# Kernel tuning notes

Measured on AMD Instinct MI355X. Metric: run time of the kernel, lower is better.

Reference implementation:

```python
import jax, jax.numpy as jnp
import numpy as np

N = 50000      # nodes
E = 800000     # edges
F_IN = 128     # input features
H = 8          # heads
F = 16         # features per head
NEG_SLOPE = 0.2


def setup_inputs() -> dict:
    key = jax.random.key(0)
    k_x, k_ei, k_w, k_as, k_ad = jax.random.split(key, 5)
    x = jax.random.normal(k_x, (N, F_IN), dtype=jnp.float32)
    edge_index = jax.random.randint(k_ei, (2, E), 0, N, dtype=jnp.int64)
    # learned params (PyG GATConv: lin weight [H*F, F_in] no bias; att_src/att_dst [H, F]; out bias [H*F])
    glorot = lambda k, shp: jax.random.uniform(k, shp, jnp.float32, -1.0, 1.0) * np.sqrt(6.0 / (shp[-1] + shp[-2]))
    W = glorot(k_w, (H * F, F_IN))
    att_src = glorot(k_as, (H, F))
    att_dst = glorot(k_ad, (H, F))
    bias = jnp.zeros((H * F,), dtype=jnp.float32)  # bias_init = zeros_
    return {"x": x, "W": W, "att_src": att_src, "att_dst": att_dst, "bias": bias, "edge_index": edge_index}


def reference(x, W, att_src, att_dst, bias, edge_index):
    # linear projection, split heads: [N, H, F]
    h = (x @ W.T).reshape(N, H, F)
    # per-node attention logits: [N, H]
    a_src = jnp.einsum('nhf,hf->nh', h, att_src)
    a_dst = jnp.einsum('nhf,hf->nh', h, att_dst)
    src, dst = edge_index[0], edge_index[1]
    # edge scores + LeakyReLU: [E, H]
    e = a_src[src] + a_dst[dst]
    e = jnp.where(e >= 0, e, NEG_SLOPE * e)
    # segment softmax over incoming edges of each dst node
    m = jax.ops.segment_max(e, dst, num_segments=N)          # [N, H]
    ex = jnp.exp(e - m[dst])                                  # [E, H]
    denom = jax.ops.segment_sum(ex, dst, num_segments=N)     # [N, H]
    alpha = ex / (denom[dst] + 1e-16)                         # [E, H]
    # weighted scatter-aggregate of source features
    msg = alpha[:, :, None] * h[src]                          # [E, H, F]
    out = jax.ops.segment_sum(msg, dst, num_segments=N)      # [N, H, F]
    return out.reshape(N, H * F) + bias
```

## Files before the change

### kernel.cpp

```cpp
#include <hip/hip_runtime.h>

#define NEG_SLOPE 0.2f
#define HEADS 8
#define FEAT 16
#define HF 128
#define FIN 128
#define BROWS 64
#define PITCH 136
#define BSHIFT 5
#define BNODES 32
#define MAXBUCK 2048
#define EPT 16
#define SCAP 20
#define CAP 1024

typedef __bf16 bf16x8 __attribute__((ext_vector_type(8)));
typedef float  f32x4  __attribute__((ext_vector_type(4)));

__device__ __forceinline__ bool detect_i64(const int* ei) {
    return (ei[1] | ei[3] | ei[5] | ei[7]) == 0;
}
__device__ __forceinline__ int load_idx(const int* ei, long long pos, bool is64) {
    return is64 ? ei[2 * pos] : ei[pos];
}

__device__ __forceinline__ float bf2f(unsigned u) { return __uint_as_float(u << 16); }

__device__ __forceinline__ unsigned short f2bf(float f) {
    unsigned u = __float_as_uint(f);
    unsigned r = u + 0x7fffu + ((u >> 16) & 1u);
    return (unsigned short)(r >> 16);
}

__global__ __launch_bounds__(256) void proj_binsort_kernel(
    const float* __restrict__ x, const float* __restrict__ W,
    const float* __restrict__ att_src, const float* __restrict__ att_dst,
    unsigned short* __restrict__ hb, float* __restrict__ a_src,
    float* __restrict__ a_dst,
    const int* __restrict__ ei, unsigned* __restrict__ ebuf,
    int* __restrict__ cnt2, int N, int E, int nb, int nsb, int PB)
{
    __shared__ __align__(16) char smem[(BROWS + FIN) * PITCH * 2];
    const int t = threadIdx.x;

    if (blockIdx.x >= PB) {
        int* lh = (int*)smem;
        const int blk = blockIdx.x - PB;
        const bool is64 = detect_i64(ei);
        const int e0 = blk * (EPT * 256);

        for (int b = t; b < nb; b += 256) lh[b] = 0;
        __syncthreads();

#pragma unroll
        for (int i = 0; i < EPT; ++i) {
            const int e = e0 + i * 256 + t;
            if (e < E) {
                const unsigned s = (unsigned)load_idx(ei, e, is64);
                const unsigned d = (unsigned)load_idx(ei, (long long)E + e, is64);
                const unsigned pk = s | (d << 16);
                const int bkt = d >> BSHIFT;
                const int ofs = atomicAdd(&lh[bkt], 1);
                if (ofs < SCAP)
                    ebuf[((size_t)bkt * nsb + blk) * SCAP + ofs] = pk;
            }
        }
        __syncthreads();
        for (int b = t; b < nb; b += 256)
            cnt2[blk * MAXBUCK + b] = min(lh[b], SCAP);
        return;
    }

    unsigned short* xs  = (unsigned short*)smem;
    unsigned short* wsl = xs + BROWS * PITCH;
    const int n0 = blockIdx.x * BROWS;

#pragma unroll
    for (int i = 0; i < 8; ++i) {
        const int f4 = i * 256 + t;
        const int r = f4 >> 5, c4 = f4 & 31;
        const int rr = (n0 + r < N) ? (n0 + r) : (N - 1);
        const float4 v = ((const float4*)(x + (size_t)rr * FIN))[c4];
        unsigned short* p = &xs[r * PITCH + c4 * 4];
        p[0] = f2bf(v.x); p[1] = f2bf(v.y); p[2] = f2bf(v.z); p[3] = f2bf(v.w);
    }
#pragma unroll
    for (int i = 0; i < 16; ++i) {
        const int f4 = i * 256 + t;
        const int r = f4 >> 5, c4 = f4 & 31;
        const float4 v = ((const float4*)(W + (size_t)r * FIN))[c4];
        unsigned short* p = &wsl[r * PITCH + c4 * 4];
        p[0] = f2bf(v.x); p[1] = f2bf(v.y); p[2] = f2bf(v.z); p[3] = f2bf(v.w);
    }
    __syncthreads();

    const int w = t >> 6, lane = t & 63;
    const int lrow = lane & 15;
    const int lk = lane >> 4;
    const int r0 = w * 16;

    f32x4 acc[8];
#pragma unroll
    for (int i = 0; i < 8; ++i) { f32x4 z = {0.f, 0.f, 0.f, 0.f}; acc[i] = z; }

#pragma unroll
    for (int ks = 0; ks < 4; ++ks) {
        const int kb = ks * 32 + lk * 8;
        const bf16x8 af = *(const bf16x8*)&xs[(r0 + lrow) * PITCH + kb];
#pragma unroll
        for (int tt = 0; tt < 8; ++tt) {
            const bf16x8 bf = *(const bf16x8*)&wsl[(tt * 16 + lrow) * PITCH + kb];
            acc[tt] = __builtin_amdgcn_mfma_f32_16x16x32_bf16(af, bf, acc[tt], 0, 0, 0);
        }
    }
    __syncthreads();

#pragma unroll
    for (int tt = 0; tt < 8; ++tt) {
#pragma unroll
        for (int rg = 0; rg < 4; ++rg) {
            const int row = r0 + lk * 4 + rg;
            const int col = tt * 16 + lrow;
            xs[row * PITCH + col] = f2bf(acc[tt][rg]);
        }
    }
    __syncthreads();

#pragma unroll
    for (int i = 0; i < 8; ++i) {
        const int u4 = i * 256 + t;
        const int r = u4 >> 5, c4 = u4 & 31;
        if (n0 + r < N) {
            const unsigned short* p = &xs[r * PITCH + c4 * 4];
            ushort4 v; v.x = p[0]; v.y = p[1]; v.z = p[2]; v.w = p[3];
            ((ushort4*)hb)[(size_t)(n0 + r) * (HF / 4) + c4] = v;
        }
    }
#pragma unroll
    for (int i = 0; i < 2; ++i) {
        const int p = i * 256 + t;
        const int r = p >> 3, hd = p & 7;
        if (n0 + r < N) {
            float s = 0.f, d = 0.f;
#pragma unroll
            for (int j = 0; j < FEAT; ++j) {
                const float hv = bf2f(xs[r * PITCH + hd * FEAT + j]);
                s = fmaf(hv, att_src[hd * FEAT + j], s);
                d = fmaf(hv, att_dst[hd * FEAT + j], d);
            }
            a_src[(size_t)(n0 + r) * HEADS + hd] = s;
            a_dst[(size_t)(n0 + r) * HEADS + hd] = d;
        }
    }
}

__global__ __launch_bounds__(256) void bucket_agg(
    const unsigned* __restrict__ ebuf, const int* __restrict__ cnt2,
    const float* __restrict__ a_src, const float* __restrict__ a_dst,
    const unsigned short* __restrict__ hb, const float* __restrict__ bias,
    float* __restrict__ out, int N, int nsb)
{
    __shared__ unsigned ubuf[CAP];
    __shared__ unsigned srt[CAP];
    __shared__ int cnts[BNODES], sc[BNODES], cur[BNODES];
    __shared__ int wsum[4];
    const int b = blockIdx.x;
    const int t = threadIdx.x;
    const int w = t >> 6, lane = t & 63;

    const int v = (t < nsb) ? cnt2[t * MAXBUCK + b] : 0;
    int x = v;
#pragma unroll
    for (int off = 1; off < 64; off <<= 1) {
        const int y = __shfl_up(x, off, 64);
        if (lane >= off) x += y;
    }
    if (lane == 63) wsum[w] = x;
    __syncthreads();
    int add = 0, tot = 0;
#pragma unroll
    for (int i = 0; i < 4; ++i) {
        const int ws_i = wsum[i];
        if (i < w) add += ws_i;
        tot += ws_i;
    }
    const int incl = x + add;
    const int myoff = incl - v;
    const int cntb = min(tot, CAP);

    if (t < nsb && v > 0) {
        const unsigned* sp = ebuf + ((size_t)b * nsb + t) * SCAP;
        for (int j = 0; j < v; ++j) {
            const int o = myoff + j;
            if (o < CAP) ubuf[o] = sp[j];
        }
    }
    if (t < BNODES) cnts[t] = 0;
    __syncthreads();

    for (int j = t; j < cntb; j += 256)
        atomicAdd(&cnts[(ubuf[j] >> 16) & (BNODES - 1)], 1);
    __syncthreads();

    if (t < BNODES) {
        const int c = cnts[t];
        int sx = c;
#pragma unroll
        for (int off = 1; off < BNODES; off <<= 1) {
            const int y = __shfl_up(sx, off, 64);
            if (t >= off) sx += y;
        }
        sc[t] = sx;
        cur[t] = sx - c;
    }
    __syncthreads();

    for (int j = t; j < cntb; j += 256) {
        const unsigned p = ubuf[j];
        const int dl = (p >> 16) & (BNODES - 1);
        const int ofs = atomicAdd(&cur[dl], 1);
        srt[ofs] = p & 0xffffu;
    }
    __syncthreads();

    const int hd = lane >> 3;
    const float2 b2 = ((const float2*)bias)[lane];

#pragma unroll 1
    for (int i = 0; i < BNODES / 4; ++i) {
        const int dl = w * (BNODES / 4) + i;
        const int d = b * BNODES + dl;
        if (d >= N) break;
        const int end = sc[dl];
        const int beg = end - cnts[dl];
        const float adh = a_dst[d * HEADS + hd];

        float acc0 = 0.f, acc1 = 0.f, den = 0.f;
        int j = beg;
        for (; j + 8 <= end; j += 8) {
            int s[8]; unsigned p[8]; float wg[8];
#pragma unroll
            for (int k = 0; k < 8; ++k) s[k] = (int)srt[j + k];
#pragma unroll
            for (int k = 0; k < 8; ++k)
                p[k] = *(const unsigned*)(hb + (size_t)s[k] * HF + 2 * lane);
#pragma unroll
            for (int k = 0; k < 8; ++k) {
                float vv = a_src[s[k] * HEADS + hd] + adh;
                vv = vv >= 0.f ? vv : NEG_SLOPE * vv;
                wg[k] = __expf(vv);
            }
#pragma unroll
            for (int k = 0; k < 8; ++k) {
                acc0 = fmaf(wg[k], bf2f(p[k] & 0xffffu), acc0);
                acc1 = fmaf(wg[k], bf2f(p[k] >> 16),     acc1);
                den += wg[k];
            }
        }
        for (; j + 4 <= end; j += 4) {
            int s[4]; unsigned p[4]; float wg[4];
#pragma unroll
            for (int k = 0; k < 4; ++k) s[k] = (int)srt[j + k];
#pragma unroll
            for (int k = 0; k < 4; ++k)
                p[k] = *(const unsigned*)(hb + (size_t)s[k] * HF + 2 * lane);
#pragma unroll
            for (int k = 0; k < 4; ++k) {
                float vv = a_src[s[k] * HEADS + hd] + adh;
                vv = vv >= 0.f ? vv : NEG_SLOPE * vv;
                wg[k] = __expf(vv);
            }
#pragma unroll
            for (int k = 0; k < 4; ++k) {
                acc0 = fmaf(wg[k], bf2f(p[k] & 0xffffu), acc0);
                acc1 = fmaf(wg[k], bf2f(p[k] >> 16),     acc1);
                den += wg[k];
            }
        }
        for (; j < end; ++j) {
            const int s = (int)srt[j];
            const unsigned p = *(const unsigned*)(hb + (size_t)s * HF + 2 * lane);
            float vv = a_src[s * HEADS + hd] + adh;
            vv = vv >= 0.f ? vv : NEG_SLOPE * vv;
            const float wg = __expf(vv);
            acc0 = fmaf(wg, bf2f(p & 0xffffu), acc0);
            acc1 = fmaf(wg, bf2f(p >> 16), acc1);
            den += wg;
        }
        const float inv = 1.f / (den + 1e-16f);
        float2 o2;
        o2.x = fmaf(acc0, inv, b2.x);
        o2.y = fmaf(acc1, inv, b2.y);
        ((float2*)out)[(size_t)d * (HF / 2) + lane] = o2;
    }
}

extern "C" void kernel_launch(void* const* d_in, const int* in_sizes, int n_in,
                              void* d_out, int out_size, void* d_ws, size_t ws_size,
                              hipStream_t stream)
{
    const float* x       = (const float*)d_in[0];
    const float* W       = (const float*)d_in[1];
    const float* att_src = (const float*)d_in[2];
    const float* att_dst = (const float*)d_in[3];
    const float* bias    = (const float*)d_in[4];
    const int*   ei      = (const int*)d_in[5];
    float* out = (float*)d_out;

    const int N = in_sizes[0] / FIN;
    const int E = in_sizes[5] / 2;
    const int NBUCK = (N + BNODES - 1) >> BSHIFT;
    const int NSB = (E + EPT * 256 - 1) / (EPT * 256);
    const int PB = (N + BROWS - 1) / BROWS;

    char* ws = (char*)d_ws;
    unsigned short* hb = (unsigned short*)ws; ws += (size_t)N * HF * 2;
    unsigned* ebuf = (unsigned*)ws; ws += (size_t)NBUCK * NSB * SCAP * 4;
    int* cnt2      = (int*)ws;  ws += (size_t)NSB * MAXBUCK * sizeof(int);
    float* a_src  = (float*)ws; ws += (size_t)N * HEADS * sizeof(float);
    float* a_dst  = (float*)ws; ws += (size_t)N * HEADS * sizeof(float);

    hipLaunchKernelGGL(proj_binsort_kernel, dim3(PB + NSB), dim3(256), 0, stream,
                       x, W, att_src, att_dst, hb, a_src, a_dst,
                       ei, ebuf, cnt2, N, E, NBUCK, NSB, PB);
    hipLaunchKernelGGL(bucket_agg, dim3(NBUCK), dim3(256), 0, stream,
                       ebuf, cnt2, a_src, a_dst, hb, bias, out, N, NSB);
}
```

Measured before the change: 157.6 us.

## Use global-atomic bucket sort and share attention exp across lanes via shuffles

Replaces the per-block sub-bucket binning (which needed a prefix-scan gather in the aggregation kernel) with a separate binsort kernel that uses global atomics to append edges straight into fixed-capacity per-bucket buffers. This adds a memset and splits projection and binning into separate launches, so they no longer overlap in one grid. In the aggregation loop, each lane now computes one (edge, head) exp weight and broadcasts it with shuffles, so it no longer evaluates 8 redundant exps and a_src loads per edge. Global atomic contention on about 1563 counters and the loss of the fused projection/binsort overlap are the added risks.

```diff
diff --git a/kernel.cpp b/kernel.cpp
--- a/kernel.cpp
+++ b/kernel.cpp
@@ -9,9 +9,6 @@
 #define PITCH 136
 #define BSHIFT 5
 #define BNODES 32
-#define MAXBUCK 2048
-#define EPT 16
-#define SCAP 20
 #define CAP 1024
 
 typedef __bf16 bf16x8 __attribute__((ext_vector_type(8)));
@@ -32,47 +29,15 @@
     return (unsigned short)(r >> 16);
 }
 
-__global__ __launch_bounds__(256) void proj_binsort_kernel(
+__global__ __launch_bounds__(256) void proj_kernel(
     const float* __restrict__ x, const float* __restrict__ W,
     const float* __restrict__ att_src, const float* __restrict__ att_dst,
     unsigned short* __restrict__ hb, float* __restrict__ a_src,
-    float* __restrict__ a_dst,
-    const int* __restrict__ ei, unsigned* __restrict__ ebuf,
-    int* __restrict__ cnt2, int N, int E, int nb, int nsb, int PB)
-{
-    __shared__ __align__(16) char smem[(BROWS + FIN) * PITCH * 2];
+    float* __restrict__ a_dst, int N)
+{
+    __shared__ __align__(16) unsigned short xs[(BROWS + FIN) * PITCH];
+    unsigned short* wsl = xs + BROWS * PITCH;
     const int t = threadIdx.x;
-
-    if (blockIdx.x >= PB) {
-        int* lh = (int*)smem;
-        const int blk = blockIdx.x - PB;
-        const bool is64 = detect_i64(ei);
-        const int e0 = blk * (EPT * 256);
-
-        for (int b = t; b < nb; b += 256) lh[b] = 0;
-        __syncthreads();
-
-#pragma unroll
-        for (int i = 0; i < EPT; ++i) {
-            const int e = e0 + i * 256 + t;
-            if (e < E) {
-                const unsigned s = (unsigned)load_idx(ei, e, is64);
-                const unsigned d = (unsigned)load_idx(ei, (long long)E + e, is64);
-                const unsigned pk = s | (d << 16);
-                const int bkt = d >> BSHIFT;
-                const int ofs = atomicAdd(&lh[bkt], 1);
-                if (ofs < SCAP)
-                    ebuf[((size_t)bkt * nsb + blk) * SCAP + ofs] = pk;
-            }
-        }
-        __syncthreads();
-        for (int b = t; b < nb; b += 256)
-            cnt2[blk * MAXBUCK + b] = min(lh[b], SCAP);
-        return;
-    }
-
-    unsigned short* xs  = (unsigned short*)smem;
-    unsigned short* wsl = xs + BROWS * PITCH;
     const int n0 = blockIdx.x * BROWS;
 
 #pragma unroll
@@ -154,47 +119,37 @@
     }
 }
 
+__global__ __launch_bounds__(256) void binsort_kernel(
+    const int* __restrict__ ei, unsigned* __restrict__ ebuf,
+    int* __restrict__ gcnt, int E)
+{
+    const bool is64 = detect_i64(ei);
+    const int stride = gridDim.x * 256;
+    for (int e = blockIdx.x * 256 + threadIdx.x; e < E; e += stride) {
+        const unsigned s = (unsigned)load_idx(ei, e, is64);
+        const unsigned d = (unsigned)load_idx(ei, (long long)E + e, is64);
+        const int bkt = (int)(d >> BSHIFT);
+        const int ofs = atomicAdd(&gcnt[bkt], 1);
+        if (ofs < CAP)
+            ebuf[(size_t)bkt * CAP + ofs] = s | (d << 16);
+    }
+}
+
 __global__ __launch_bounds__(256) void bucket_agg(
-    const unsigned* __restrict__ ebuf, const int* __restrict__ cnt2,
+    const unsigned* __restrict__ ebuf, const int* __restrict__ gcnt,
     const float* __restrict__ a_src, const float* __restrict__ a_dst,
     const unsigned short* __restrict__ hb, const float* __restrict__ bias,
-    float* __restrict__ out, int N, int nsb)
+    float* __restrict__ out, int N)
 {
     __shared__ unsigned ubuf[CAP];
     __shared__ unsigned srt[CAP];
     __shared__ int cnts[BNODES], sc[BNODES], cur[BNODES];
-    __shared__ int wsum[4];
     const int b = blockIdx.x;
     const int t = threadIdx.x;
     const int w = t >> 6, lane = t & 63;
 
-    const int v = (t < nsb) ? cnt2[t * MAXBUCK + b] : 0;
-    int x = v;
-#pragma unroll
-    for (int off = 1; off < 64; off <<= 1) {
-        const int y = __shfl_up(x, off, 64);
-        if (lane >= off) x += y;
-    }
-    if (lane == 63) wsum[w] = x;
-    __syncthreads();
-    int add = 0, tot = 0;
-#pragma unroll
-    for (int i = 0; i < 4; ++i) {
-        const int ws_i = wsum[i];
-        if (i < w) add += ws_i;
-        tot += ws_i;
-    }
-    const int incl = x + add;
-    const int myoff = incl - v;
-    const int cntb = min(tot, CAP);
-
-    if (t < nsb && v > 0) {
-        const unsigned* sp = ebuf + ((size_t)b * nsb + t) * SCAP;
-        for (int j = 0; j < v; ++j) {
-            const int o = myoff + j;
-            if (o < CAP) ubuf[o] = sp[j];
-        }
-    }
+    const int cntb = min(gcnt[b], CAP);
+    for (int j = t; j < cntb; j += 256) ubuf[j] = ebuf[(size_t)b * CAP + j];
     if (t < BNODES) cnts[t] = 0;
     __syncthreads();
 
@@ -223,7 +178,8 @@
     }
     __syncthreads();
 
-    const int hd = lane >> 3;
+    const int hd  = lane >> 3;
+    const int h_w = lane & 7;
     const float2 b2 = ((const float2*)bias)[lane];
 
 #pragma unroll 1
@@ -233,7 +189,7 @@
         if (d >= N) break;
         const int end = sc[dl];
         const int beg = end - cnts[dl];
-        const float adh = a_dst[d * HEADS + hd];
+        const float adh_w = a_dst[d * HEADS + h_w];
 
         float acc0 = 0.f, acc1 = 0.f, den = 0.f;
         int j = beg;
@@ -244,12 +200,12 @@
 #pragma unroll
             for (int k = 0; k < 8; ++k)
                 p[k] = *(const unsigned*)(hb + (size_t)s[k] * HF + 2 * lane);
-#pragma unroll
-            for (int k = 0; k < 8; ++k) {
-                float vv = a_src[s[k] * HEADS + hd] + adh;
-                vv = vv >= 0.f ? vv : NEG_SLOPE * vv;
-                wg[k] = __expf(vv);
-            }
+            const int sw = (int)srt[j + (lane >> 3)];
+            float vv = a_src[sw * HEADS + h_w] + adh_w;
+            vv = vv >= 0.f ? vv : NEG_SLOPE * vv;
+            const float wv = __expf(vv);
+#pragma unroll
+            for (int k = 0; k < 8; ++k) wg[k] = __shfl(wv, (k << 3) | hd, 64);
 #pragma unroll
             for (int k = 0; k < 8; ++k) {
                 acc0 = fmaf(wg[k], bf2f(p[k] & 0xffffu), acc0);
@@ -264,12 +220,12 @@
 #pragma unroll
             for (int k = 0; k < 4; ++k)
                 p[k] = *(const unsigned*)(hb + (size_t)s[k] * HF + 2 * lane);
-#pragma unroll
-            for (int k = 0; k < 4; ++k) {
-                float vv = a_src[s[k] * HEADS + hd] + adh;
-                vv = vv >= 0.f ? vv : NEG_SLOPE * vv;
-                wg[k] = __expf(vv);
-            }
+            const int sw = (int)srt[j + ((lane >> 3) & 3)];
+            float vv = a_src[sw * HEADS + h_w] + adh_w;
+            vv = vv >= 0.f ? vv : NEG_SLOPE * vv;
+            const float wv = __expf(vv);
+#pragma unroll
+            for (int k = 0; k < 4; ++k) wg[k] = __shfl(wv, (k << 3) | hd, 64);
 #pragma unroll
             for (int k = 0; k < 4; ++k) {
                 acc0 = fmaf(wg[k], bf2f(p[k] & 0xffffu), acc0);
@@ -280,9 +236,10 @@
         for (; j < end; ++j) {
             const int s = (int)srt[j];
             const unsigned p = *(const unsigned*)(hb + (size_t)s * HF + 2 * lane);
-            float vv = a_src[s * HEADS + hd] + adh;
+            float vv = a_src[s * HEADS + h_w] + adh_w;
             vv = vv >= 0.f ? vv : NEG_SLOPE * vv;
-            const float wg = __expf(vv);
+            const float wv = __expf(vv);
+            const float wg = __shfl(wv, hd, 64);
             acc0 = fmaf(wg, bf2f(p & 0xffffu), acc0);
             acc1 = fmaf(wg, bf2f(p >> 16), acc1);
             den += wg;
@@ -310,19 +267,20 @@
     const int N = in_sizes[0] / FIN;
     const int E = in_sizes[5] / 2;
     const int NBUCK = (N + BNODES - 1) >> BSHIFT;
-    const int NSB = (E + EPT * 256 - 1) / (EPT * 256);
     const int PB = (N + BROWS - 1) / BROWS;
 
     char* ws = (char*)d_ws;
     unsigned short* hb = (unsigned short*)ws; ws += (size_t)N * HF * 2;
-    unsigned* ebuf = (unsigned*)ws; ws += (size_t)NBUCK * NSB * SCAP * 4;
-    int* cnt2      = (int*)ws;  ws += (size_t)NSB * MAXBUCK * sizeof(int);
+    unsigned* ebuf = (unsigned*)ws; ws += (size_t)NBUCK * CAP * 4;
+    int* gcnt      = (int*)ws;  ws += (size_t)NBUCK * sizeof(int);
     float* a_src  = (float*)ws; ws += (size_t)N * HEADS * sizeof(float);
     float* a_dst  = (float*)ws; ws += (size_t)N * HEADS * sizeof(float);
 
-    hipLaunchKernelGGL(proj_binsort_kernel, dim3(PB + NSB), dim3(256), 0, stream,
-                       x, W, att_src, att_dst, hb, a_src, a_dst,
-                       ei, ebuf, cnt2, N, E, NBUCK, NSB, PB);
+    hipMemsetAsync(gcnt, 0, (size_t)NBUCK * sizeof(int), stream);
+    hipLaunchKernelGGL(binsort_kernel, dim3(2048), dim3(256), 0, stream,
+                       ei, ebuf, gcnt, E);
+    hipLaunchKernelGGL(proj_kernel, dim3(PB), dim3(256), 0, stream,
+                       x, W, att_src, att_dst, hb, a_src, a_dst, N);
     hipLaunchKernelGGL(bucket_agg, dim3(NBUCK), dim3(256), 0, stream,
-                       ebuf, cnt2, a_src, a_dst, hb, bias, out, N, NSB);
-}
+                       ebuf, gcnt, a_src, a_dst, hb, bias, out, N);
+}
```

New measurement: 260.6 us. +65.4%, slower.
